# Optimization experiments

Measured on AMD Instinct MI355X. Metric: run time of the kernel, lower is better.

## Reference

```python
import jax, jax.numpy as jnp
import numpy as np

B, T1, T2, V, D, H = 128, 256, 256, 50000, 300, 300


def _lstm_dir(x, lens, Wih, Whh, bih, bhh):
    # PyTorch LSTM gate order: i, f, g, o. Length-masked scan emulates pack_padded_sequence:
    # state frozen and outputs zeroed for t >= len.
    Bn, T, _ = x.shape
    Hn = Whh.shape[1]
    mask = (jnp.arange(T)[None, :] < lens[:, None]).astype(x.dtype)[..., None]  # [B,T,1]

    def step(carry, inp):
        h, c = carry
        xt, mt = inp
        gates = xt @ Wih.T + bih + h @ Whh.T + bhh
        i, f, g, o = jnp.split(gates, 4, axis=-1)
        c_new = jax.nn.sigmoid(f) * c + jax.nn.sigmoid(i) * jnp.tanh(g)
        h_new = jax.nn.sigmoid(o) * jnp.tanh(c_new)
        h = mt * h_new + (1.0 - mt) * h
        c = mt * c_new + (1.0 - mt) * c
        return (h, c), h * mt

    init = (jnp.zeros((Bn, Hn), x.dtype), jnp.zeros((Bn, Hn), x.dtype))
    _, ys = jax.lax.scan(step, init, (x.swapaxes(0, 1), mask.swapaxes(0, 1)))
    return ys.swapaxes(0, 1)  # [B,T,H]


def _bilstm(x, lens, Wf_ih, Wf_hh, bf_ih, bf_hh, Wb_ih, Wb_hh, bb_ih, bb_hh):
    out_f = _lstm_dir(x, lens, Wf_ih, Wf_hh, bf_ih, bf_hh)
    T = x.shape[1]
    t = jnp.arange(T)[None, :]
    # per-sample reversal of the valid prefix (involution): rev[t] = l-1-t for t<l else t
    idx = jnp.where(t < lens[:, None], lens[:, None] - 1 - t, t)
    xr = jnp.take_along_axis(x, idx[..., None], axis=1)
    yr = _lstm_dir(xr, lens, Wb_ih, Wb_hh, bb_ih, bb_hh)
    out_b = jnp.take_along_axis(yr, idx[..., None], axis=1)
    return jnp.concatenate([out_f, out_b], axis=-1)  # [B,T,2H]


def _bidaf_both(u1, l1, u2, l2):
    S = jnp.einsum('bid,bjd->bij', u1, u2)  # [B,t1,t2]
    v1 = jnp.arange(S.shape[1])[None, :] < l1[:, None]
    v2 = jnp.arange(S.shape[2])[None, :] < l2[:, None]
    Sm = jnp.where(v1[:, :, None] & v2[:, None, :], S, -1e9)
    # softmax over t2 (s1->s2 attention); invalid rows zeroed (matches NaN->0 fill)
    a2 = jax.nn.softmax(Sm, axis=2) * v1[:, :, None].astype(S.dtype)
    a1 = jax.nn.softmax(Sm, axis=1) * v2[:, None, :].astype(S.dtype)
    U = jnp.einsum('bij,bjd->bid', a2, u2)   # tile for s1
    U1 = jnp.einsum('bij,bid->bjd', a1, u1)  # tile for s2
    return U, U1


def _max_along_time(x, lens):
    v = jnp.arange(x.shape[1])[None, :] < lens[:, None]
    return jnp.max(jnp.where(v[:, :, None], x, -jnp.inf), axis=1)


def _forward(s1, l1, s2, l2, emb,
             w1f_ih, w1f_hh, b1f_ih, b1f_hh, w1b_ih, w1b_hh, b1b_ih, b1b_hh,
             w2f_ih, w2f_hh, b2f_ih, b2f_hh, w2b_ih, w2b_hh, b2b_ih, b2b_hh,
             projW, projB, mlpW, mlpB, smW, smB):
    p1 = emb[s1]  # [B,T1,D]
    p2 = emb[s2]
    u1 = _bilstm(p1, l1, w1f_ih, w1f_hh, b1f_ih, b1f_hh, w1b_ih, w1b_hh, b1b_ih, b1b_hh)
    u2 = _bilstm(p2, l2, w1f_ih, w1f_hh, b1f_ih, b1f_hh, w1b_ih, w1b_hh, b1b_ih, b1b_hh)
    A1, A2 = _bidaf_both(u1, l1, u2, l2)
    c1 = jnp.concatenate([u1, A1, u1 - A1, u1 * A1], axis=-1)  # [B,T1,8H]
    c2 = jnp.concatenate([u2, A2, u2 - A2, u2 * A2], axis=-1)
    p1c = jax.nn.relu(c1 @ projW.T + projB)
    p2c = jax.nn.relu(c2 @ projW.T + projB)
    y1 = _bilstm(p1c, l1, w2f_ih, w2f_hh, b2f_ih, b2f_hh, w2b_ih, w2b_hh, b2b_ih, b2b_hh)
    y2 = _bilstm(p2c, l2, w2f_ih, w2f_hh, b2f_ih, b2f_hh, w2b_ih, w2b_hh, b2b_ih, b2b_hh)
    m1 = _max_along_time(y1, l1)  # [B,2H]
    m2 = _max_along_time(y2, l2)
    feat = jnp.concatenate([m1, m2, jnp.abs(m1 - m2), m1 * m2], axis=-1)  # [B,8H]
    h = jax.nn.relu(feat @ mlpW.T + mlpB)
    return h @ smW.T + smB  # [B,3]


def setup_inputs():
    key = jax.random.key(0)
    ks = jax.random.split(key, 24)
    sc = 0.05
    W = lambda i, shape: jax.random.normal(ks[i], shape, jnp.float32) * sc
    return dict(
        s1=jax.random.randint(ks[0], (B, T1), 0, V),
        l1=jax.random.randint(ks[1], (B,), 1, T1 + 1),
        s2=jax.random.randint(ks[2], (B, T2), 0, V),
        l2=jax.random.randint(ks[3], (B,), 1, T2 + 1),
        emb=W(4, (V, D)),
        w1f_ih=W(5, (4 * H, D)), w1f_hh=W(6, (4 * H, H)), b1f_ih=W(7, (4 * H,)), b1f_hh=W(8, (4 * H,)),
        w1b_ih=W(9, (4 * H, D)), w1b_hh=W(10, (4 * H, H)), b1b_ih=W(11, (4 * H,)), b1b_hh=W(12, (4 * H,)),
        w2f_ih=W(13, (4 * H, H)), w2f_hh=W(14, (4 * H, H)), b2f_ih=W(15, (4 * H,)), b2f_hh=W(16, (4 * H,)),
        w2b_ih=W(17, (4 * H, H)), w2b_hh=W(18, (4 * H, H)), b2b_ih=W(19, (4 * H,)), b2b_hh=W(20, (4 * H,)),
        projW=W(21, (H, 8 * H)), projB=jnp.zeros((H,), jnp.float32),
        mlpW=W(22, (300, 8 * H)), mlpB=jnp.zeros((300,), jnp.float32),
        smW=W(23, (3, 300)), smB=jnp.zeros((3,), jnp.float32),
    )


def reference(s1, l1, s2, l2, emb,
              w1f_ih, w1f_hh, b1f_ih, b1f_hh, w1b_ih, w1b_hh, b1b_ih, b1b_hh,
              w2f_ih, w2f_hh, b2f_ih, b2f_hh, w2b_ih, w2b_hh, b2b_ih, b2b_hh,
              projW, projB, mlpW, mlpB, smW, smB):
    return _forward(s1, l1, s2, l2, emb,
                    w1f_ih, w1f_hh, b1f_ih, b1f_hh, w1b_ih, w1b_hh, b1b_ih, b1b_hh,
                    w2f_ih, w2f_hh, b2f_ih, b2f_hh, w2b_ih, w2b_hh, b2b_ih, b2b_hh,
                    projW, projB, mlpW, mlpB, smW, smB)
```

## Files before the change

### kernel.cpp

```cpp
#include <hip/hip_runtime.h>
#include <hip/hip_bf16.h>


typedef unsigned short u16;
typedef float fx4 __attribute__((ext_vector_type(4)));
typedef short s16x8 __attribute__((ext_vector_type(8)));

__device__ __forceinline__ float us2f(u16 u){
  unsigned int x = ((unsigned int)u) << 16;
  float f; __builtin_memcpy(&f, &x, 4); return f;
}
__device__ __forceinline__ u16 f2us(float f){
  unsigned int x; __builtin_memcpy(&x, &f, 4);
  unsigned int r = x + 0x7fffu + ((x >> 16) & 1u);
  return (u16)(r >> 16);
}
__device__ __forceinline__ float sigmf(float x){ return 1.0f/(1.0f + __expf(-x)); }
__device__ __forceinline__ float tanhfast(float x){ return 1.0f - 2.0f/(__expf(2.0f*x) + 1.0f); }

__global__ __launch_bounds__(256) void k_embed(const int* __restrict__ s1, const int* __restrict__ s2,
                                               const float* __restrict__ emb, u16* __restrict__ p)
{
  int id = blockIdx.x*256 + threadIdx.x;
  if (id >= 65536*75) return;
  int row = id / 75;
  int c4 = (id - row*75) * 4;
  int tok = (row < 32768) ? s1[row] : s2[row - 32768];
  float4 v = *(const float4*)(emb + (size_t)tok*300 + c4);
  ushort4 o; o.x=f2us(v.x); o.y=f2us(v.y); o.z=f2us(v.z); o.w=f2us(v.w);
  *(ushort4*)(p + (size_t)row*300 + c4) = o;
}

__global__ __launch_bounds__(256) void k_cvt(const float* __restrict__ in, u16* __restrict__ out, int n)
{
  int id = blockIdx.x*256 + threadIdx.x;
  if (id < n) out[id] = f2us(in[id]);
}

__global__ __launch_bounds__(256) void k_pack(const float* __restrict__ W, u16* __restrict__ pack)
{
  int id = blockIdx.x*256 + threadIdx.x;
  if (id >= 51200) return;
  const int lane = id & 63;
  const int kt2 = (id >> 6) % 10;
  const int nt2 = id / 640;
  const int n = nt2*16 + (lane & 15);
  u16 tmp[8];
#pragma unroll
  for (int j = 0; j < 8; ++j){
    const int k = kt2*32 + (lane >> 4)*8 + j;
    tmp[j] = (n < 1200 && k < 300) ? f2us(W[(size_t)n*300 + k]) : (u16)0;
  }
  *(s16x8*)(pack + (size_t)id*8) = *(const s16x8*)tmp;
}

__global__ __launch_bounds__(256) void k_mm_xpc(
    const u16* __restrict__ A,
    const u16* __restrict__ WFb, const u16* __restrict__ WBb,
    const float* __restrict__ bF1, const float* __restrict__ bF2,
    const float* __restrict__ bB1, const float* __restrict__ bB2,
    const int* __restrict__ l1, const int* __restrict__ l2,
    u16* __restrict__ xp, int c)
{
  const int dir = blockIdx.z;
  const u16* Bw = dir ? WBb : WFb;
  const float* b1 = dir ? bB1 : bF1;
  const float* b2 = dir ? bB2 : bF2;
  u16* xpd = xp + (size_t)dir*9830400;
  __shared__ u16 As[128][40];
  __shared__ u16 Bs[128][40];
  const int tid = threadIdx.x;
  const int m0 = blockIdx.y << 7;
  const int n0 = blockIdx.x << 7;
  const int srow0 = tid >> 2;
  const int kcol = (tid & 3) << 3;
  int src[2];
#pragma unroll
  for (int p = 0; p < 2; ++p){
    const int row = srow0 + (p << 6);
    const int ml = m0 + row;
    const int r = ml >> 5, tl = ml & 31;
    const int L = (r < 128) ? l1[r] : l2[r-128];
    const int tg = (c << 5) + tl;
    const int s = dir ? ((tg < L) ? (L-1-tg) : tg) : tg;
    src[p] = r*256 + s;
  }
  const int wv = tid >> 6;
  const int wm = (wv >> 1) << 6, wn = (wv & 1) << 6;
  const int lq = (tid >> 4) & 3;
  const int lr = tid & 15;
  fx4 acc[4][4];
#pragma unroll
  for (int i = 0; i < 4; ++i)
#pragma unroll
    for (int j = 0; j < 4; ++j) acc[i][j] = (fx4){0.f,0.f,0.f,0.f};

  for (int kt = 0; kt < 10; ++kt){
    const int k = (kt << 5) + kcol;
#pragma unroll
    for (int p = 0; p < 2; ++p){
      u16 tmp[8];
      const u16* ap = A + (size_t)src[p]*300 + k;
      if (k + 8 <= 300){
        *(ushort4*)&tmp[0] = *(const ushort4*)ap;
        *(ushort4*)&tmp[4] = *(const ushort4*)(ap + 4);
      } else {
#pragma unroll
        for (int j = 0; j < 8; ++j) tmp[j] = (k + j < 300) ? ap[j] : (u16)0;
      }
      *(s16x8*)&As[srow0 + (p << 6)][kcol] = *(const s16x8*)tmp;

      const int n = n0 + srow0 + (p << 6);
      u16 tmb[8] = {0,0,0,0,0,0,0,0};
      if (n < 1200){
        const u16* bp = Bw + (size_t)n*300 + k;
        if (k + 8 <= 300){
          *(ushort4*)&tmb[0] = *(const ushort4*)bp;
          *(ushort4*)&tmb[4] = *(const ushort4*)(bp + 4);
        } else {
#pragma unroll
          for (int j = 0; j < 8; ++j) tmb[j] = (k + j < 300) ? bp[j] : (u16)0;
        }
      }
      *(s16x8*)&Bs[srow0 + (p << 6)][kcol] = *(const s16x8*)tmb;
    }
    __syncthreads();
    s16x8 af[4], bf[4];
#pragma unroll
    for (int mi = 0; mi < 4; ++mi) af[mi] = *(const s16x8*)&As[wm + mi*16 + lr][lq << 3];
#pragma unroll
    for (int ni = 0; ni < 4; ++ni) bf[ni] = *(const s16x8*)&Bs[wn + ni*16 + lr][lq << 3];
#pragma unroll
    for (int mi = 0; mi < 4; ++mi)
#pragma unroll
      for (int ni = 0; ni < 4; ++ni)
        acc[mi][ni] = __builtin_amdgcn_mfma_f32_16x16x32_bf16(af[mi], bf[ni], acc[mi][ni], 0, 0, 0);
    __syncthreads();
  }
#pragma unroll
  for (int ni = 0; ni < 4; ++ni){
    const int n = n0 + wn + ni*16 + lr;
    if (n < 1200){
      const float bias = b1[n] + b2[n];
#pragma unroll
      for (int mi = 0; mi < 4; ++mi){
        const int m = m0 + wm + mi*16 + (lq << 2);
#pragma unroll
        for (int reg = 0; reg < 4; ++reg)
          xpd[(size_t)(m + reg)*1200 + n] = f2us(acc[mi][ni][reg] + bias);
      }
    }
  }
}

__global__ __launch_bounds__(256) void k_mm_s(const u16* __restrict__ U, float* __restrict__ S)
{
  __shared__ u16 As[128][40];
  __shared__ u16 Bs[128][40];
  const int tid = threadIdx.x;
  const int bz = blockIdx.z;
  const u16* Ap = U + (size_t)bz*153600;
  const u16* Bp = U + (size_t)(128+bz)*153600;
  float* C = S + (size_t)bz*65536;
  const int m0 = blockIdx.y << 7;
  const int n0 = blockIdx.x << 7;
  const int srow0 = tid >> 2;
  const int kcol = (tid & 3) << 3;
  const int wv = tid >> 6;
  const int wm = (wv >> 1) << 6, wn = (wv & 1) << 6;
  const int lq = (tid >> 4) & 3;
  const int lr = tid & 15;
  fx4 acc[4][4];
#pragma unroll
  for (int i = 0; i < 4; ++i)
#pragma unroll
    for (int j = 0; j < 4; ++j) acc[i][j] = (fx4){0.f,0.f,0.f,0.f};

  for (int kt = 0; kt < 19; ++kt){
    const int k = (kt << 5) + kcol;
#pragma unroll
    for (int p = 0; p < 2; ++p){
      const int row = srow0 + (p << 6);
      u16 tma[8] = {0,0,0,0,0,0,0,0};
      u16 tmb[8] = {0,0,0,0,0,0,0,0};
      if (k + 8 <= 600){
        *(s16x8*)tma = *(const s16x8*)(Ap + (size_t)(m0 + row)*600 + k);
        *(s16x8*)tmb = *(const s16x8*)(Bp + (size_t)(n0 + row)*600 + k);
      }
      *(s16x8*)&As[row][kcol] = *(const s16x8*)tma;
      *(s16x8*)&Bs[row][kcol] = *(const s16x8*)tmb;
    }
    __syncthreads();
    s16x8 af[4], bf[4];
#pragma unroll
    for (int mi = 0; mi < 4; ++mi) af[mi] = *(const s16x8*)&As[wm + mi*16 + lr][lq << 3];
#pragma unroll
    for (int ni = 0; ni < 4; ++ni) bf[ni] = *(const s16x8*)&Bs[wn + ni*16 + lr][lq << 3];
#pragma unroll
    for (int mi = 0; mi < 4; ++mi)
#pragma unroll
      for (int ni = 0; ni < 4; ++ni)
        acc[mi][ni] = __builtin_amdgcn_mfma_f32_16x16x32_bf16(af[mi], bf[ni], acc[mi][ni], 0, 0, 0);
    __syncthreads();
  }
#pragma unroll
  for (int mi = 0; mi < 4; ++mi){
    const int m = m0 + wm + mi*16 + (lq << 2);
#pragma unroll
    for (int ni = 0; ni < 4; ++ni){
      const int n = n0 + wn + ni*16 + lr;
#pragma unroll
      for (int reg = 0; reg < 4; ++reg)
        C[(size_t)(m + reg)*256 + n] = acc[mi][ni][reg];
    }
  }
}

__global__ __launch_bounds__(256) void k_mm_proj(
    const u16* __restrict__ U, const u16* __restrict__ ATT,
    const u16* __restrict__ Bw,
    const float* __restrict__ bias,
    u16* __restrict__ C)
{
  __shared__ u16 As0[128][40];
  __shared__ u16 As1[128][40];
  __shared__ u16 Bs0[128][40];
  __shared__ u16 Bs1[128][40];
  const int tid = threadIdx.x;
  const int id = ((int)(blockIdx.x & 7))*192 + ((int)blockIdx.x >> 3);
  const int mg = id / 3, nb = id - mg*3;
  const int m0 = mg << 7, n0 = nb << 7;
  const int srow0 = tid >> 2;
  const int kcol = (tid & 3) << 3;
  const int wv = tid >> 6;
  const int wm = (wv >> 1) << 6, wn = (wv & 1) << 6;
  const int lq = (tid >> 4) & 3;
  const int lr = tid & 15;
  fx4 acc[4][4];
#pragma unroll
  for (int i = 0; i < 4; ++i)
#pragma unroll
    for (int j = 0; j < 4; ++j) acc[i][j] = (fx4){0.f,0.f,0.f,0.f};

  for (int kt = 0; kt < 19; ++kt){
    const int off = (kt << 5) + kcol;
    const bool ok = (off < 600);
#pragma unroll
    for (int p = 0; p < 2; ++p){
      const int row = srow0 + (p << 6);
      u16 u8[8] = {0,0,0,0,0,0,0,0};
      u16 a8[8] = {0,0,0,0,0,0,0,0};
      if (ok){
        *(s16x8*)u8 = *(const s16x8*)(U   + (size_t)(m0+row)*600 + off);
        *(s16x8*)a8 = *(const s16x8*)(ATT + (size_t)(m0+row)*600 + off);
      }
      *(s16x8*)&As0[row][kcol] = *(const s16x8*)u8;
      *(s16x8*)&As1[row][kcol] = *(const s16x8*)a8;
      const int n = n0 + row;
      u16 w0[8] = {0,0,0,0,0,0,0,0};
      u16 w1[8] = {0,0,0,0,0,0,0,0};
      if (n < 300 && ok){
        *(s16x8*)w0 = *(const s16x8*)(Bw + (size_t)n*2400 + off);
        *(s16x8*)w1 = *(const s16x8*)(Bw + (size_t)n*2400 + 600 + off);
      }
      *(s16x8*)&Bs0[row][kcol] = *(const s16x8*)w0;
      *(s16x8*)&Bs1[row][kcol] = *(const s16x8*)w1;
    }
    __syncthreads();
    {
      s16x8 af0[4], af1[4], bf0[4], bf1[4];
#pragma unroll
      for (int mi = 0; mi < 4; ++mi){
        af0[mi] = *(const s16x8*)&As0[wm + mi*16 + lr][lq << 3];
        af1[mi] = *(const s16x8*)&As1[wm + mi*16 + lr][lq << 3];
      }
#pragma unroll
      for (int ni = 0; ni < 4; ++ni){
        bf0[ni] = *(const s16x8*)&Bs0[wn + ni*16 + lr][lq << 3];
        bf1[ni] = *(const s16x8*)&Bs1[wn + ni*16 + lr][lq << 3];
      }
#pragma unroll
      for (int mi = 0; mi < 4; ++mi)
#pragma unroll
        for (int ni = 0; ni < 4; ++ni){
          acc[mi][ni] = __builtin_amdgcn_mfma_f32_16x16x32_bf16(af0[mi], bf0[ni], acc[mi][ni], 0, 0, 0);
          acc[mi][ni] = __builtin_amdgcn_mfma_f32_16x16x32_bf16(af1[mi], bf1[ni], acc[mi][ni], 0, 0, 0);
        }
    }
    __syncthreads();
#pragma unroll
    for (int p = 0; p < 2; ++p){
      const int row = srow0 + (p << 6);
      u16 u8[8] = {0,0,0,0,0,0,0,0};
      u16 a8[8] = {0,0,0,0,0,0,0,0};
      if (ok){
        *(s16x8*)u8 = *(const s16x8*)(U   + (size_t)(m0+row)*600 + off);
        *(s16x8*)a8 = *(const s16x8*)(ATT + (size_t)(m0+row)*600 + off);
      }
      u16 d8[8], m8[8];
#pragma unroll
      for (int j = 0; j < 8; ++j){
        const float uf = us2f(u8[j]), af = us2f(a8[j]);
        d8[j] = f2us(uf - af);
        m8[j] = f2us(uf * af);
      }
      *(s16x8*)&As0[row][kcol] = *(const s16x8*)d8;
      *(s16x8*)&As1[row][kcol] = *(const s16x8*)m8;
      const int n = n0 + row;
      u16 w2[8] = {0,0,0,0,0,0,0,0};
      u16 w3[8] = {0,0,0,0,0,0,0,0};
      if (n < 300 && ok){
        *(s16x8*)w2 = *(const s16x8*)(Bw + (size_t)n*2400 + 1200 + off);
        *(s16x8*)w3 = *(const s16x8*)(Bw + (size_t)n*2400 + 1800 + off);
      }
      *(s16x8*)&Bs0[row][kcol] = *(const s16x8*)w2;
      *(s16x8*)&Bs1[row][kcol] = *(const s16x8*)w3;
    }
    __syncthreads();
    {
      s16x8 af0[4], af1[4], bf0[4], bf1[4];
#pragma unroll
      for (int mi = 0; mi < 4; ++mi){
        af0[mi] = *(const s16x8*)&As0[wm + mi*16 + lr][lq << 3];
        af1[mi] = *(const s16x8*)&As1[wm + mi*16 + lr][lq << 3];
      }
#pragma unroll
      for (int ni = 0; ni < 4; ++ni){
        bf0[ni] = *(const s16x8*)&Bs0[wn + ni*16 + lr][lq << 3];
        bf1[ni] = *(const s16x8*)&Bs1[wn + ni*16 + lr][lq << 3];
      }
#pragma unroll
      for (int mi = 0; mi < 4; ++mi)
#pragma unroll
        for (int ni = 0; ni < 4; ++ni){
          acc[mi][ni] = __builtin_amdgcn_mfma_f32_16x16x32_bf16(af0[mi], bf0[ni], acc[mi][ni], 0, 0, 0);
          acc[mi][ni] = __builtin_amdgcn_mfma_f32_16x16x32_bf16(af1[mi], bf1[ni], acc[mi][ni], 0, 0, 0);
        }
    }
    __syncthreads();
  }
#pragma unroll
  for (int ni = 0; ni < 4; ++ni){
    const int n = n0 + wn + ni*16 + lr;
    if (n < 300){
      const float bs = bias[n];
#pragma unroll
      for (int mi = 0; mi < 4; ++mi){
        const int m = m0 + wm + mi*16 + (lq << 2);
#pragma unroll
        for (int reg = 0; reg < 4; ++reg)
          C[(size_t)(m + reg)*300 + n] = f2us(fmaxf(acc[mi][ni][reg] + bs, 0.0f));
      }
    }
  }
}

__global__ __launch_bounds__(512) void k_scan_mf(
    const u16* __restrict__ xp,
    const u16* __restrict__ packF, const u16* __restrict__ packB,
    const int* __restrict__ l1, const int* __restrict__ l2,
    u16* __restrict__ uo,
    u16* __restrict__ hG, float* __restrict__ cG,
    int c)
{
  __shared__ u16 h_pack[10][64][8];
  __shared__ float gs[8][1200];
  __shared__ u16 wring[8][3][4][512];
  __shared__ int L_s[8];
  const int bid = blockIdx.x;
  const int dir = bid & 1, sg = bid >> 1;
  const int r0 = sg << 3;
  const u16* pack = dir ? packB : packF;
  const u16* xpd = xp + (size_t)dir*9830400;
  const int tid = threadIdx.x;
  if (tid < 8) L_s[tid] = (r0 + tid < 128) ? l1[r0 + tid] : l2[r0 + tid - 128];
  for (int i = tid; i < 10*64*8; i += 512) ((u16*)h_pack)[i] = 0;
  __syncthreads();
  if (c > 0){
    for (int i = tid; i < 2400; i += 512){
      const int q = i / 300, d = i - q*300;
      h_pack[d >> 5][(((d & 31) >> 3) << 4) | q][d & 7] =
          hG[(size_t)(dir*256 + r0 + q)*328 + d];
    }
  }
  int q_[5], d_[5]; bool v_[5];
#pragma unroll
  for (int j = 0; j < 5; ++j){
    const int u0 = tid + (j << 9);
    v_[j] = (u0 < 2400);
    const int qq = v_[j] ? (u0 / 300) : 0;
    q_[j] = qq;
    d_[j] = v_[j] ? (u0 - qq*300) : 0;
  }
  float c_reg[5];
#pragma unroll
  for (int j = 0; j < 5; ++j)
    c_reg[j] = (v_[j] && c > 0) ? cG[(size_t)(dir*256 + r0 + q_[j])*304 + d_[j]] : 0.0f;
  __syncthreads();

  int Lmax = 0;
#pragma unroll
  for (int q = 0; q < 8; ++q) Lmax = max(Lmax, L_s[q]);
  const int t0 = c << 5;
  int nts = Lmax - t0; if (nts > 32) nts = 32;
  if (nts <= 0) return;

  const int w = tid >> 6, lane = tid & 63;
  const int lq = lane >> 4, lr = lane & 15;
  const int tile0 = w * 10;
  const u16* pw = pack + (size_t)tile0*5120;
  const unsigned wb0 = (unsigned)(uintptr_t)&wring[w][0][0][0] + (unsigned)lane*16u;

#define WISSUE(FB, BUF)                                                                  \
  {                                                                                      \
    _Pragma("unroll")                                                                    \
    for (int i2 = 0; i2 < 4; ++i2){                                                      \
      const int f_ = (FB) + i2;                                                          \
      const u16* ga = pw + ((size_t)(((f_ % 10)*10) + (f_ / 10)))*512 + (size_t)lane*8;  \
      __builtin_amdgcn_global_load_lds(                                                  \
        (const __attribute__((address_space(1))) void*)ga,                               \
        (__attribute__((address_space(3))) void*)&wring[w][BUF][i2][0], 16, 0, 0);       \
    }                                                                                    \
  }

  WISSUE(0, 0)
  WISSUE(4, 1)
  int rot = 0;

  for (int tl = 0; tl < nts; ++tl){
    const int t = t0 + tl;
    const int bsel0 = rot;
    const int bsel1 = (rot + 1 == 3) ? 0 : rot + 1;
    const int bsel2 = (rot + 2 >= 3) ? rot - 1 : rot + 2;
    const int bsel[3] = { bsel0, bsel1, bsel2 };
    __builtin_amdgcn_sched_barrier(0);
    u16 xg0[5], xg1[5], xg2[5], xg3[5];
#pragma unroll
    for (int j = 0; j < 5; ++j){
      const size_t base = (size_t)((r0 + q_[j])*32 + tl)*1200 + d_[j];
      xg0[j] = v_[j] ? xpd[base      ] : (u16)0;
      xg1[j] = v_[j] ? xpd[base + 300] : (u16)0;
      xg2[j] = v_[j] ? xpd[base + 600] : (u16)0;
      xg3[j] = v_[j] ? xpd[base + 900] : (u16)0;
    }
    __builtin_amdgcn_sched_barrier(0);

    fx4 acc[10];
#pragma unroll
    for (int nt = 0; nt < 10; ++nt) acc[nt] = (fx4){0.f,0.f,0.f,0.f};

#pragma unroll
    for (int p = 0; p < 25; ++p){
      if (p < 2){ asm volatile("s_waitcnt vmcnt(24)" ::: "memory"); }
      else      { asm volatile("s_waitcnt vmcnt(4)"  ::: "memory"); }
      __builtin_amdgcn_sched_barrier(0);
      const unsigned ab = wb0 + (unsigned)bsel[p % 3]*4096u;
      s16x8 b0, b1, b2, b3;
      asm volatile("ds_read_b128 %0, %1"             : "=v"(b0) : "v"(ab));
      asm volatile("ds_read_b128 %0, %1 offset:1024" : "=v"(b1) : "v"(ab));
      asm volatile("ds_read_b128 %0, %1 offset:2048" : "=v"(b2) : "v"(ab));
      asm volatile("ds_read_b128 %0, %1 offset:3072" : "=v"(b3) : "v"(ab));
      const int kt0 = (4*p) / 10;
      const int kt3 = (4*p + 3) / 10;
      const s16x8 a0 = *(const s16x8*)&h_pack[kt0][lane][0];
      const s16x8 a1 = (kt3 != kt0) ? *(const s16x8*)&h_pack[kt3][lane][0] : a0;
      WISSUE((((p + 2) % 25) * 4), bsel[(p + 2) % 3])
      asm volatile("s_waitcnt lgkmcnt(0)" ::: "memory");
      __builtin_amdgcn_sched_barrier(0);
      {
        const int f0 = 4*p;
        acc[(f0+0) % 10] = __builtin_amdgcn_mfma_f32_16x16x32_bf16(((f0+0)/10 == kt0) ? a0 : a1, b0, acc[(f0+0) % 10], 0, 0, 0);
        acc[(f0+1) % 10] = __builtin_amdgcn_mfma_f32_16x16x32_bf16(((f0+1)/10 == kt0) ? a0 : a1, b1, acc[(f0+1) % 10], 0, 0, 0);
        acc[(f0+2) % 10] = __builtin_amdgcn_mfma_f32_16x16x32_bf16(((f0+2)/10 == kt0) ? a0 : a1, b2, acc[(f0+2) % 10], 0, 0, 0);
        acc[(f0+3) % 10] = __builtin_amdgcn_mfma_f32_16x16x32_bf16(((f0+3)/10 == kt0) ? a0 : a1, b3, acc[(f0+3) % 10], 0, 0, 0);
      }
    }
    rot = (rot + 1 == 3) ? 0 : rot + 1;

    if (lq < 2){
#pragma unroll
      for (int nt = 0; nt < 10; ++nt){
        const int n = (tile0 + nt)*16 + lr;
        if (n < 1200){
#pragma unroll
          for (int reg = 0; reg < 4; ++reg)
            gs[(lq << 2) + reg][n] = acc[nt][reg];
        }
      }
    }
    asm volatile("s_waitcnt lgkmcnt(0)" ::: "memory");
    __builtin_amdgcn_sched_barrier(0);
    __builtin_amdgcn_s_barrier();
#pragma unroll
    for (int j = 0; j < 5; ++j){
      if (v_[j]){
        const int q = q_[j], d = d_[j];
        const int L = L_s[q];
        if (t < L){
          const float gi = gs[q][d]       + us2f(xg0[j]);
          const float gf = gs[q][300 + d] + us2f(xg1[j]);
          const float gg = gs[q][600 + d] + us2f(xg2[j]);
          const float go = gs[q][900 + d] + us2f(xg3[j]);
          const float cn = sigmf(gf)*c_reg[j] + sigmf(gi)*tanhfast(gg);
          const float hn = sigmf(go)*tanhfast(cn);
          c_reg[j] = cn;
          const u16 hb = f2us(hn);
          h_pack[d >> 5][(((d & 31) >> 3) << 4) | q][d & 7] = hb;
          const int wpos = dir ? (L-1-t) : t;
          uo[(size_t)((r0 + q)*256 + wpos)*600 + dir*300 + d] = hb;
        }
      }
    }
    asm volatile("s_waitcnt lgkmcnt(0)" ::: "memory");
    __builtin_amdgcn_sched_barrier(0);
    __builtin_amdgcn_s_barrier();
  }
#undef WISSUE
  for (int i = tid; i < 2400; i += 512){
    const int q = i / 300, d = i - q*300;
    hG[(size_t)(dir*256 + r0 + q)*328 + d] =
        h_pack[d >> 5][(((d & 31) >> 3) << 4) | q][d & 7];
  }
#pragma unroll
  for (int j = 0; j < 5; ++j)
    if (v_[j]) cG[(size_t)(dir*256 + r0 + q_[j])*304 + d_[j]] = c_reg[j];
}

__global__ __launch_bounds__(256) void k_row_stats(const float* __restrict__ S, const int* __restrict__ l2,
                                                   float* __restrict__ rmax, float* __restrict__ rinv)
{
  const int wid = threadIdx.x >> 6, lane = threadIdx.x & 63;
  const int row = blockIdx.x*4 + wid;
  const int b = row >> 8;
  const int L2b = l2[b];
  float4 v = *(const float4*)(S + (size_t)row*256 + lane*4);
  const int j = lane*4;
  float m = -INFINITY;
  if (j   < L2b) m = fmaxf(m, v.x);
  if (j+1 < L2b) m = fmaxf(m, v.y);
  if (j+2 < L2b) m = fmaxf(m, v.z);
  if (j+3 < L2b) m = fmaxf(m, v.w);
  for (int off = 32; off; off >>= 1) m = fmaxf(m, __shfl_xor(m, off));
  float s = 0.f;
  if (j   < L2b) s += __expf(v.x - m);
  if (j+1 < L2b) s += __expf(v.y - m);
  if (j+2 < L2b) s += __expf(v.z - m);
  if (j+3 < L2b) s += __expf(v.w - m);
  for (int off = 32; off; off >>= 1) s += __shfl_xor(s, off);
  if (lane == 0){ rmax[row] = m; rinv[row] = 1.0f/s; }
}

__global__ __launch_bounds__(256) void k_col_stats(const float* __restrict__ S, const int* __restrict__ l1,
                                                   float* __restrict__ cmax, float* __restrict__ cinv)
{
  const int b = blockIdx.x;
  const int j = threadIdx.x;
  const int L1b = l1[b];
  const float* Sb = S + (size_t)b*65536;
  float m = -INFINITY;
  for (int i = 0; i < L1b; ++i) m = fmaxf(m, Sb[(size_t)i*256 + j]);
  float s = 0.f;
  for (int i = 0; i < L1b; ++i) s += __expf(Sb[(size_t)i*256 + j] - m);
  cmax[b*256 + j] = m;
  cinv[b*256 + j] = 1.0f/s;
}

__global__ __launch_bounds__(256) void k_av_row(
    const float* __restrict__ S, const u16* __restrict__ U,
    const int* __restrict__ l1, const int* __restrict__ l2,
    const float* __restrict__ rmax, const float* __restrict__ rinv,
    u16* __restrict__ ATT)
{
  __shared__ float Ps[32][68];
  __shared__ float Us[32][68];
  const int tid = threadIdx.x;
  const int b = blockIdx.z;
  const int i0 = blockIdx.y << 6;
  const int d0 = blockIdx.x << 6;
  const int L1b = l1[b], L2b = l2[b];
  const float* Sb = S + (size_t)b*65536;
  const u16* u2 = U + (size_t)(128+b)*153600;
  const int tx = tid & 15, ty = tid >> 4;
  float acc[4][4];
#pragma unroll
  for (int i = 0; i < 4; ++i)
#pragma unroll
    for (int j = 0; j < 4; ++j) acc[i][j] = 0.0f;

  for (int kt = 0; kt < 8; ++kt){
    const int j0 = kt << 5;
#pragma unroll
    for (int q = 0; q < 2; ++q){
      const int f4 = tid + (q << 8);
      {
        const int row = f4 >> 3;
        const int c4 = (f4 & 7) << 2;
        const int i = i0 + row;
        float4 s4 = *(const float4*)(Sb + (size_t)i*256 + j0 + c4);
        const float rm = rmax[(b<<8) + i];
        const float ri = rinv[(b<<8) + i];
        const int jb = j0 + c4;
        Ps[c4  ][row] = (jb   < L2b) ? __expf(s4.x - rm)*ri : 0.0f;
        Ps[c4+1][row] = (jb+1 < L2b) ? __expf(s4.y - rm)*ri : 0.0f;
        Ps[c4+2][row] = (jb+2 < L2b) ? __expf(s4.z - rm)*ri : 0.0f;
        Ps[c4+3][row] = (jb+3 < L2b) ? __expf(s4.w - rm)*ri : 0.0f;
      }
      {
        const int row = f4 >> 4;
        const int c4 = (f4 & 15) << 2;
        const int d = d0 + c4;
        float4 v = make_float4(0.f,0.f,0.f,0.f);
        if (j0 + row < L2b){
          const u16* up = u2 + (size_t)(j0+row)*600 + d;
          if (d + 3 < 600){
            ushort4 t4 = *(const ushort4*)up;
            v.x=us2f(t4.x); v.y=us2f(t4.y); v.z=us2f(t4.z); v.w=us2f(t4.w);
          } else {
            if (d   < 600) v.x = us2f(up[0]);
            if (d+1 < 600) v.y = us2f(up[1]);
            if (d+2 < 600) v.z = us2f(up[2]);
          }
        }
        *(float4*)&Us[row][c4] = v;
      }
    }
    __syncthreads();
#pragma unroll
    for (int kk = 0; kk < 32; ++kk){
      float4 a = *(const float4*)&Ps[kk][ty<<2];
      float4 bb = *(const float4*)&Us[kk][tx<<2];
      float av[4] = {a.x,a.y,a.z,a.w};
      float bv[4] = {bb.x,bb.y,bb.z,bb.w};
#pragma unroll
      for (int ii = 0; ii < 4; ++ii)
#pragma unroll
        for (int jj = 0; jj < 4; ++jj)
          acc[ii][jj] = fmaf(av[ii], bv[jj], acc[ii][jj]);
    }
    __syncthreads();
  }
#pragma unroll
  for (int ii = 0; ii < 4; ++ii){
    const int i = i0 + (ty<<2) + ii;
#pragma unroll
    for (int jj = 0; jj < 4; ++jj){
      const int d = d0 + (tx<<2) + jj;
      if (d < 600)
        ATT[(size_t)b*153600 + (size_t)i*600 + d] = f2us((i < L1b) ? acc[ii][jj] : 0.0f);
    }
  }
}

__global__ __launch_bounds__(256) void k_av_col(
    const float* __restrict__ S, const u16* __restrict__ U,
    const int* __restrict__ l1, const int* __restrict__ l2,
    const float* __restrict__ cmax, const float* __restrict__ cinv,
    u16* __restrict__ ATT)
{
  __shared__ float Ps[32][68];
  __shared__ float Us[32][68];
  const int tid = threadIdx.x;
  const int b = blockIdx.z;
  const int j0v = blockIdx.y << 6;
  const int d0 = blockIdx.x << 6;
  const int L1b = l1[b], L2b = l2[b];
  const float* Sb = S + (size_t)b*65536;
  const u16* u1 = U + (size_t)b*153600;
  const int tx = tid & 15, ty = tid >> 4;
  float acc[4][4];
#pragma unroll
  for (int i = 0; i < 4; ++i)
#pragma unroll
    for (int j = 0; j < 4; ++j) acc[i][j] = 0.0f;

  for (int kt = 0; kt < 8; ++kt){
    const int i0k = kt << 5;
#pragma unroll
    for (int q = 0; q < 2; ++q){
      const int f4 = tid + (q << 8);
      const int row = f4 >> 4;
      const int c4 = (f4 & 15) << 2;
      {
        const int i = i0k + row;
        const int j = j0v + c4;
        float4 s4 = *(const float4*)(Sb + (size_t)i*256 + j);
        const bool iok = i < L1b;
        Ps[row][c4  ] = iok ? __expf(s4.x - cmax[(b<<8)+j  ])*cinv[(b<<8)+j  ] : 0.0f;
        Ps[row][c4+1] = iok ? __expf(s4.y - cmax[(b<<8)+j+1])*cinv[(b<<8)+j+1] : 0.0f;
        Ps[row][c4+2] = iok ? __expf(s4.z - cmax[(b<<8)+j+2])*cinv[(b<<8)+j+2] : 0.0f;
        Ps[row][c4+3] = iok ? __expf(s4.w - cmax[(b<<8)+j+3])*cinv[(b<<8)+j+3] : 0.0f;
      }
      {
        const int d = d0 + c4;
        float4 v = make_float4(0.f,0.f,0.f,0.f);
        if (i0k + row < L1b){
          const u16* up = u1 + (size_t)(i0k+row)*600 + d;
          if (d + 3 < 600){
            ushort4 t4 = *(const ushort4*)up;
            v.x=us2f(t4.x); v.y=us2f(t4.y); v.z=us2f(t4.z); v.w=us2f(t4.w);
          } else {
            if (d   < 600) v.x = us2f(up[0]);
            if (d+1 < 600) v.y = us2f(up[1]);
            if (d+2 < 600) v.z = us2f(up[2]);
          }
        }
        *(float4*)&Us[row][c4] = v;
      }
    }
    __syncthreads();
#pragma unroll
    for (int kk = 0; kk < 32; ++kk){
      float4 a = *(const float4*)&Ps[kk][ty<<2];
      float4 bb = *(const float4*)&Us[kk][tx<<2];
      float av[4] = {a.x,a.y,a.z,a.w};
      float bv[4] = {bb.x,bb.y,bb.z,bb.w};
#pragma unroll
      for (int ii = 0; ii < 4; ++ii)
#pragma unroll
        for (int jj = 0; jj < 4; ++jj)
          acc[ii][jj] = fmaf(av[ii], bv[jj], acc[ii][jj]);
    }
    __syncthreads();
  }
#pragma unroll
  for (int ii = 0; ii < 4; ++ii){
    const int j = j0v + (ty<<2) + ii;
#pragma unroll
    for (int jj = 0; jj < 4; ++jj){
      const int d = d0 + (tx<<2) + jj;
      if (d < 600)
        ATT[(size_t)(128+b)*153600 + (size_t)j*600 + d] = f2us((j < L2b) ? acc[ii][jj] : 0.0f);
    }
  }
}

__global__ __launch_bounds__(256) void k_maxfeat(const u16* __restrict__ y,
                                                 const int* __restrict__ l1, const int* __restrict__ l2,
                                                 float* __restrict__ feat)
{
  const int b = blockIdx.x;
  const int La = l1[b], Lb = l2[b];
  for (int c = threadIdx.x; c < 600; c += 256){
    float m1 = -INFINITY, m2 = -INFINITY;
    const u16* y1 = y + (size_t)b*153600 + c;
    for (int t = 0; t < La; ++t) m1 = fmaxf(m1, us2f(y1[(size_t)t*600]));
    const u16* y2 = y + (size_t)(128+b)*153600 + c;
    for (int t = 0; t < Lb; ++t) m2 = fmaxf(m2, us2f(y2[(size_t)t*600]));
    feat[(size_t)b*2400 + c]        = m1;
    feat[(size_t)b*2400 + 600 + c]  = m2;
    feat[(size_t)b*2400 + 1200 + c] = fabsf(m1 - m2);
    feat[(size_t)b*2400 + 1800 + c] = m1*m2;
  }
}

__global__ __launch_bounds__(256) void k_rowgemm(const float* __restrict__ feat, const float* __restrict__ W,
                                                 const float* __restrict__ bias, float* __restrict__ out)
{
  const int b = blockIdx.x;
  __shared__ float ff[2400];
  for (int i = threadIdx.x; i < 2400; i += 256) ff[i] = feat[(size_t)b*2400 + i];
  __syncthreads();
  for (int n = threadIdx.x; n < 300; n += 256){
    const float* w = W + (size_t)n*2400;
    float acc = bias[n];
    for (int k = 0; k < 2400; k += 4){
      float4 wv = *(const float4*)(w + k);
      acc += ff[k]*wv.x + ff[k+1]*wv.y + ff[k+2]*wv.z + ff[k+3]*wv.w;
    }
    out[(size_t)b*300 + n] = fmaxf(acc, 0.0f);
  }
}

__global__ __launch_bounds__(192) void k_final(const float* __restrict__ h, const float* __restrict__ smW,
                                               const float* __restrict__ smB, float* __restrict__ out)
{
  const int b = blockIdx.x;
  const int n = threadIdx.x >> 6, lane = threadIdx.x & 63;
  float acc = 0.f;
  for (int k = lane; k < 300; k += 64) acc += h[(size_t)b*300 + k]*smW[(size_t)n*300 + k];
  for (int off = 32; off; off >>= 1) acc += __shfl_xor(acc, off);
  if (lane == 0) out[b*3 + n] = acc + smB[n];
}

extern "C" void kernel_launch(void* const* d_in, const int* in_sizes, int n_in,
                              void* d_out, int out_size, void* d_ws, size_t ws_size,
                              hipStream_t stream)
{
  (void)in_sizes; (void)n_in; (void)out_size;
  static const size_t OFF_P  = 0;
  static const size_t OFF_B  = 39321600;
  static const size_t OFF_U  = 78643200;
  static const size_t OFF_D  = 157286400;
  static const size_t OFF_WT = 235929600;
  static const size_t OFF_PJ = 238809600;
  static const size_t OFF_PK = 240249600;
  static const size_t OFF_ST = 243526400;
  static const size_t OFF_FE = 244050688;
  static const size_t OFF_HM = 245279488;
  static const size_t OFF_HC = 245433088;
  static const size_t WS_NEEDED = 246391552;
  if (ws_size < WS_NEEDED) return;

  const int* s1 = (const int*)d_in[0];
  const int* l1 = (const int*)d_in[1];
  const int* s2 = (const int*)d_in[2];
  const int* l2 = (const int*)d_in[3];
  const float* emb    = (const float*)d_in[4];
  const float* w1f_ih = (const float*)d_in[5];
  const float* w1f_hh = (const float*)d_in[6];
  const float* b1f_ih = (const float*)d_in[7];
  const float* b1f_hh = (const float*)d_in[8];
  const float* w1b_ih = (const float*)d_in[9];
  const float* w1b_hh = (const float*)d_in[10];
  const float* b1b_ih = (const float*)d_in[11];
  const float* b1b_hh = (const float*)d_in[12];
  const float* w2f_ih = (const float*)d_in[13];
  const float* w2f_hh = (const float*)d_in[14];
  const float* b2f_ih = (const float*)d_in[15];
  const float* b2f_hh = (const float*)d_in[16];
  const float* w2b_ih = (const float*)d_in[17];
  const float* w2b_hh = (const float*)d_in[18];
  const float* b2b_ih = (const float*)d_in[19];
  const float* b2b_hh = (const float*)d_in[20];
  const float* projW  = (const float*)d_in[21];
  const float* projB  = (const float*)d_in[22];
  const float* mlpW   = (const float*)d_in[23];
  const float* mlpB   = (const float*)d_in[24];
  const float* smW    = (const float*)d_in[25];
  const float* smB    = (const float*)d_in[26];

  char* ws = (char*)d_ws;
  u16*   p    = (u16*)(ws + OFF_P);
  u16*   xp1  = (u16*)(ws + OFF_B);
  float* Smat = (float*)(ws + OFF_B);
  u16*   pc   = (u16*)(ws + OFF_B);
  u16*   uu   = (u16*)(ws + OFF_U);
  u16*   att  = (u16*)(ws + OFF_D);
  u16*   xp2  = (u16*)(ws + OFF_D);
  u16*   wih  = (u16*)(ws + OFF_WT);
  u16*   pjw  = (u16*)(ws + OFF_PJ);
  u16*   pk   = (u16*)(ws + OFF_PK);
  float* st   = (float*)(ws + OFF_ST);
  float* feat = (float*)(ws + OFF_FE);
  float* hml  = (float*)(ws + OFF_HM);
  u16*   hG   = (u16*)(ws + OFF_HC);
  float* cG   = (float*)(ws + OFF_HC + 335872);

  k_embed<<<19200, 256, 0, stream>>>(s1, s2, emb, p);
  k_cvt<<<1407, 256, 0, stream>>>(w1f_ih, wih,           360000);
  k_cvt<<<1407, 256, 0, stream>>>(w1b_ih, wih + 360000,  360000);
  k_cvt<<<1407, 256, 0, stream>>>(w2f_ih, wih + 720000,  360000);
  k_cvt<<<1407, 256, 0, stream>>>(w2b_ih, wih + 1080000, 360000);
  k_cvt<<<2813, 256, 0, stream>>>(projW,  pjw,           720000);
  k_pack<<<200, 256, 0, stream>>>(w1f_hh, pk);
  k_pack<<<200, 256, 0, stream>>>(w1b_hh, pk + 409600);
  k_pack<<<200, 256, 0, stream>>>(w2f_hh, pk + 819200);
  k_pack<<<200, 256, 0, stream>>>(w2b_hh, pk + 1228800);

  const dim3 gxp(10, 64, 2);
  for (int c = 0; c < 8; ++c){
    k_mm_xpc<<<gxp, 256, 0, stream>>>(p, wih, wih + 360000, b1f_ih, b1f_hh, b1b_ih, b1b_hh,
                                      l1, l2, xp1, c);
    k_scan_mf<<<64, 512, 0, stream>>>(xp1, pk, pk + 409600, l1, l2, uu, hG, cG, c);
  }

  k_mm_s<<<dim3(2,2,128), 256, 0, stream>>>(uu, Smat);
  k_row_stats<<<8192, 256, 0, stream>>>(Smat, l2, st, st + 32768);
  k_col_stats<<<128, 256, 0, stream>>>(Smat, l1, st + 65536, st + 98304);
  k_av_row<<<dim3(10,4,128), 256, 0, stream>>>(Smat, uu, l1, l2, st, st + 32768, att);
  k_av_col<<<dim3(10,4,128), 256, 0, stream>>>(Smat, uu, l1, l2, st + 65536, st + 98304, att);

  k_mm_proj<<<1536, 256, 0, stream>>>(uu, att, pjw, projB, pc);

  for (int c = 0; c < 8; ++c){
    k_mm_xpc<<<gxp, 256, 0, stream>>>(pc, wih + 720000, wih + 1080000, b2f_ih, b2f_hh, b2b_ih, b2b_hh,
                                      l1, l2, xp2, c);
    k_scan_mf<<<64, 512, 0, stream>>>(xp2, pk + 819200, pk + 1228800, l1, l2, uu, hG, cG, c);
  }

  k_maxfeat<<<128, 256, 0, stream>>>(uu, l1, l2, feat);
  k_rowgemm<<<128, 256, 0, stream>>>(feat, mlpW, mlpB, hml);
  k_final<<<128, 192, 0, stream>>>(hml, smW, smB, (float*)d_out);
}
```

Before: 9.869 ms.

## Process 16 rows per scan block with 1024 threads and register-streamed weights

The recurrent LSTM scan now handles 16 sequences per block, filling all 16 MFMA M-rows instead of 8. It uses 1024 threads across 16 waves, each covering 5 gate tiles instead of 10, and launches half as many blocks. The LDS weight ring fed by global_load_lds is removed, and recurrent weights are loaded straight from global into registers with a two-stage register double buffer. The input-projection loads move from a prefetch ahead of the MFMA loop into the gate update. The aim is to halve per-row weight traffic and shorten the serial MFMA chain per step, at the cost of exposing global-load latency each timestep and using fewer CUs.

```diff
diff --git a/kernel.cpp b/kernel.cpp
--- a/kernel.cpp
+++ b/kernel.cpp
@@ -355,7 +355,7 @@
   }
 }
 
-__global__ __launch_bounds__(512) void k_scan_mf(
+__global__ __launch_bounds__(1024) void k_scan_mf(
     const u16* __restrict__ xp,
     const u16* __restrict__ packF, const u16* __restrict__ packB,
     const int* __restrict__ l1, const int* __restrict__ l2,
@@ -364,143 +364,100 @@
     int c)
 {
   __shared__ u16 h_pack[10][64][8];
-  __shared__ float gs[8][1200];
-  __shared__ u16 wring[8][3][4][512];
-  __shared__ int L_s[8];
+  __shared__ float gs[16][1200];
+  __shared__ int L_s[16];
   const int bid = blockIdx.x;
   const int dir = bid & 1, sg = bid >> 1;
-  const int r0 = sg << 3;
+  const int r0 = sg << 4;
   const u16* pack = dir ? packB : packF;
   const u16* xpd = xp + (size_t)dir*9830400;
   const int tid = threadIdx.x;
-  if (tid < 8) L_s[tid] = (r0 + tid < 128) ? l1[r0 + tid] : l2[r0 + tid - 128];
-  for (int i = tid; i < 10*64*8; i += 512) ((u16*)h_pack)[i] = 0;
+  if (tid < 16) L_s[tid] = (r0 + tid < 128) ? l1[r0 + tid] : l2[r0 + tid - 128];
+  for (int i = tid; i < 10*64*8; i += 1024) ((u16*)h_pack)[i] = 0;
   __syncthreads();
   if (c > 0){
-    for (int i = tid; i < 2400; i += 512){
+    for (int i = tid; i < 4800; i += 1024){
       const int q = i / 300, d = i - q*300;
       h_pack[d >> 5][(((d & 31) >> 3) << 4) | q][d & 7] =
           hG[(size_t)(dir*256 + r0 + q)*328 + d];
     }
   }
-  int q_[5], d_[5]; bool v_[5];
+  float c_reg[5];
 #pragma unroll
   for (int j = 0; j < 5; ++j){
-    const int u0 = tid + (j << 9);
-    v_[j] = (u0 < 2400);
-    const int qq = v_[j] ? (u0 / 300) : 0;
-    q_[j] = qq;
-    d_[j] = v_[j] ? (u0 - qq*300) : 0;
-  }
-  float c_reg[5];
-#pragma unroll
-  for (int j = 0; j < 5; ++j)
-    c_reg[j] = (v_[j] && c > 0) ? cG[(size_t)(dir*256 + r0 + q_[j])*304 + d_[j]] : 0.0f;
+    const int u0 = tid + (j << 10);
+    float v = 0.0f;
+    if (u0 < 4800 && c > 0){
+      const int q = u0 / 300, d = u0 - q*300;
+      v = cG[(size_t)(dir*256 + r0 + q)*304 + d];
+    }
+    c_reg[j] = v;
+  }
   __syncthreads();
-
   int Lmax = 0;
 #pragma unroll
-  for (int q = 0; q < 8; ++q) Lmax = max(Lmax, L_s[q]);
+  for (int q = 0; q < 16; ++q) Lmax = max(Lmax, L_s[q]);
   const int t0 = c << 5;
   int nts = Lmax - t0; if (nts > 32) nts = 32;
   if (nts <= 0) return;
 
   const int w = tid >> 6, lane = tid & 63;
   const int lq = lane >> 4, lr = lane & 15;
-  const int tile0 = w * 10;
-  const u16* pw = pack + (size_t)tile0*5120;
-  const unsigned wb0 = (unsigned)(uintptr_t)&wring[w][0][0][0] + (unsigned)lane*16u;
-
-#define WISSUE(FB, BUF)                                                                  \
-  {                                                                                      \
-    _Pragma("unroll")                                                                    \
-    for (int i2 = 0; i2 < 4; ++i2){                                                      \
-      const int f_ = (FB) + i2;                                                          \
-      const u16* ga = pw + ((size_t)(((f_ % 10)*10) + (f_ / 10)))*512 + (size_t)lane*8;  \
-      __builtin_amdgcn_global_load_lds(                                                  \
-        (const __attribute__((address_space(1))) void*)ga,                               \
-        (__attribute__((address_space(3))) void*)&wring[w][BUF][i2][0], 16, 0, 0);       \
-    }                                                                                    \
-  }
-
-  WISSUE(0, 0)
-  WISSUE(4, 1)
-  int rot = 0;
+  const int tile0 = w * 5;
+  const u16* pw = pack + (size_t)tile0*5120 + (size_t)lane*8;
 
   for (int tl = 0; tl < nts; ++tl){
     const int t = t0 + tl;
-    const int bsel0 = rot;
-    const int bsel1 = (rot + 1 == 3) ? 0 : rot + 1;
-    const int bsel2 = (rot + 2 >= 3) ? rot - 1 : rot + 2;
-    const int bsel[3] = { bsel0, bsel1, bsel2 };
-    __builtin_amdgcn_sched_barrier(0);
-    u16 xg0[5], xg1[5], xg2[5], xg3[5];
+    fx4 acc[5];
+#pragma unroll
+    for (int i = 0; i < 5; ++i) acc[i] = (fx4){0.f,0.f,0.f,0.f};
+    s16x8 wA[5], wB[5];
+#pragma unroll
+    for (int i = 0; i < 5; ++i) wA[i] = *(const s16x8*)(pw + (size_t)(i*10 + 0)*512);
+#pragma unroll
+    for (int ktp = 0; ktp < 5; ++ktp){
+      const int ktE = 2*ktp, ktO = ktE + 1;
+#pragma unroll
+      for (int i = 0; i < 5; ++i) wB[i] = *(const s16x8*)(pw + (size_t)(i*10 + ktO)*512);
+      {
+        const s16x8 a = *(const s16x8*)&h_pack[ktE][lane][0];
+#pragma unroll
+        for (int i = 0; i < 5; ++i)
+          acc[i] = __builtin_amdgcn_mfma_f32_16x16x32_bf16(a, wA[i], acc[i], 0, 0, 0);
+      }
+      if (ktp < 4){
+#pragma unroll
+        for (int i = 0; i < 5; ++i) wA[i] = *(const s16x8*)(pw + (size_t)(i*10 + ktE + 2)*512);
+      }
+      {
+        const s16x8 a = *(const s16x8*)&h_pack[ktO][lane][0];
+#pragma unroll
+        for (int i = 0; i < 5; ++i)
+          acc[i] = __builtin_amdgcn_mfma_f32_16x16x32_bf16(a, wB[i], acc[i], 0, 0, 0);
+      }
+    }
+#pragma unroll
+    for (int i = 0; i < 5; ++i){
+      const int n = (tile0 + i)*16 + lr;
+      if (n < 1200){
+#pragma unroll
+        for (int reg = 0; reg < 4; ++reg)
+          gs[(lq << 2) + reg][n] = acc[i][reg];
+      }
+    }
+    __syncthreads();
 #pragma unroll
     for (int j = 0; j < 5; ++j){
-      const size_t base = (size_t)((r0 + q_[j])*32 + tl)*1200 + d_[j];
-      xg0[j] = v_[j] ? xpd[base      ] : (u16)0;
-      xg1[j] = v_[j] ? xpd[base + 300] : (u16)0;
-      xg2[j] = v_[j] ? xpd[base + 600] : (u16)0;
-      xg3[j] = v_[j] ? xpd[base + 900] : (u16)0;
-    }
-    __builtin_amdgcn_sched_barrier(0);
-
-    fx4 acc[10];
-#pragma unroll
-    for (int nt = 0; nt < 10; ++nt) acc[nt] = (fx4){0.f,0.f,0.f,0.f};
-
-#pragma unroll
-    for (int p = 0; p < 25; ++p){
-      if (p < 2){ asm volatile("s_waitcnt vmcnt(24)" ::: "memory"); }
-      else      { asm volatile("s_waitcnt vmcnt(4)"  ::: "memory"); }
-      __builtin_amdgcn_sched_barrier(0);
-      const unsigned ab = wb0 + (unsigned)bsel[p % 3]*4096u;
-      s16x8 b0, b1, b2, b3;
-      asm volatile("ds_read_b128 %0, %1"             : "=v"(b0) : "v"(ab));
-      asm volatile("ds_read_b128 %0, %1 offset:1024" : "=v"(b1) : "v"(ab));
-      asm volatile("ds_read_b128 %0, %1 offset:2048" : "=v"(b2) : "v"(ab));
-      asm volatile("ds_read_b128 %0, %1 offset:3072" : "=v"(b3) : "v"(ab));
-      const int kt0 = (4*p) / 10;
-      const int kt3 = (4*p + 3) / 10;
-      const s16x8 a0 = *(const s16x8*)&h_pack[kt0][lane][0];
-      const s16x8 a1 = (kt3 != kt0) ? *(const s16x8*)&h_pack[kt3][lane][0] : a0;
-      WISSUE((((p + 2) % 25) * 4), bsel[(p + 2) % 3])
-      asm volatile("s_waitcnt lgkmcnt(0)" ::: "memory");
-      __builtin_amdgcn_sched_barrier(0);
-      {
-        const int f0 = 4*p;
-        acc[(f0+0) % 10] = __builtin_amdgcn_mfma_f32_16x16x32_bf16(((f0+0)/10 == kt0) ? a0 : a1, b0, acc[(f0+0) % 10], 0, 0, 0);
-        acc[(f0+1) % 10] = __builtin_amdgcn_mfma_f32_16x16x32_bf16(((f0+1)/10 == kt0) ? a0 : a1, b1, acc[(f0+1) % 10], 0, 0, 0);
-        acc[(f0+2) % 10] = __builtin_amdgcn_mfma_f32_16x16x32_bf16(((f0+2)/10 == kt0) ? a0 : a1, b2, acc[(f0+2) % 10], 0, 0, 0);
-        acc[(f0+3) % 10] = __builtin_amdgcn_mfma_f32_16x16x32_bf16(((f0+3)/10 == kt0) ? a0 : a1, b3, acc[(f0+3) % 10], 0, 0, 0);
-      }
-    }
-    rot = (rot + 1 == 3) ? 0 : rot + 1;
-
-    if (lq < 2){
-#pragma unroll
-      for (int nt = 0; nt < 10; ++nt){
-        const int n = (tile0 + nt)*16 + lr;
-        if (n < 1200){
-#pragma unroll
-          for (int reg = 0; reg < 4; ++reg)
-            gs[(lq << 2) + reg][n] = acc[nt][reg];
-        }
-      }
-    }
-    asm volatile("s_waitcnt lgkmcnt(0)" ::: "memory");
-    __builtin_amdgcn_sched_barrier(0);
-    __builtin_amdgcn_s_barrier();
-#pragma unroll
-    for (int j = 0; j < 5; ++j){
-      if (v_[j]){
-        const int q = q_[j], d = d_[j];
+      const int u0 = tid + (j << 10);
+      if (u0 < 4800){
+        const int q = u0 / 300, d = u0 - q*300;
         const int L = L_s[q];
         if (t < L){
-          const float gi = gs[q][d]       + us2f(xg0[j]);
-          const float gf = gs[q][300 + d] + us2f(xg1[j]);
-          const float gg = gs[q][600 + d] + us2f(xg2[j]);
-          const float go = gs[q][900 + d] + us2f(xg3[j]);
+          const size_t xb = (size_t)((r0 + q)*32 + tl)*1200 + d;
+          const float gi = gs[q][d]       + us2f(xpd[xb      ]);
+          const float gf = gs[q][300 + d] + us2f(xpd[xb + 300]);
+          const float gg = gs[q][600 + d] + us2f(xpd[xb + 600]);
+          const float go = gs[q][900 + d] + us2f(xpd[xb + 900]);
           const float cn = sigmf(gf)*c_reg[j] + sigmf(gi)*tanhfast(gg);
           const float hn = sigmf(go)*tanhfast(cn);
           c_reg[j] = cn;
@@ -511,19 +468,21 @@
         }
       }
     }
-    asm volatile("s_waitcnt lgkmcnt(0)" ::: "memory");
-    __builtin_amdgcn_sched_barrier(0);
-    __builtin_amdgcn_s_barrier();
-  }
-#undef WISSUE
-  for (int i = tid; i < 2400; i += 512){
+    __syncthreads();
+  }
+  for (int i = tid; i < 4800; i += 1024){
     const int q = i / 300, d = i - q*300;
     hG[(size_t)(dir*256 + r0 + q)*328 + d] =
         h_pack[d >> 5][(((d & 31) >> 3) << 4) | q][d & 7];
   }
 #pragma unroll
-  for (int j = 0; j < 5; ++j)
-    if (v_[j]) cG[(size_t)(dir*256 + r0 + q_[j])*304 + d_[j]] = c_reg[j];
+  for (int j = 0; j < 5; ++j){
+    const int u0 = tid + (j << 10);
+    if (u0 < 4800){
+      const int q = u0 / 300, d = u0 - q*300;
+      cG[(size_t)(dir*256 + r0 + q)*304 + d] = c_reg[j];
+    }
+  }
 }
 
 __global__ __launch_bounds__(256) void k_row_stats(const float* __restrict__ S, const int* __restrict__ l2,
@@ -861,7 +820,7 @@
   for (int c = 0; c < 8; ++c){
     k_mm_xpc<<<gxp, 256, 0, stream>>>(p, wih, wih + 360000, b1f_ih, b1f_hh, b1b_ih, b1b_hh,
                                       l1, l2, xp1, c);
-    k_scan_mf<<<64, 512, 0, stream>>>(xp1, pk, pk + 409600, l1, l2, uu, hG, cG, c);
+    k_scan_mf<<<32, 1024, 0, stream>>>(xp1, pk, pk + 409600, l1, l2, uu, hG, cG, c);
   }
 
   k_mm_s<<<dim3(2,2,128), 256, 0, stream>>>(uu, Smat);
@@ -875,7 +834,7 @@
   for (int c = 0; c < 8; ++c){
     k_mm_xpc<<<gxp, 256, 0, stream>>>(pc, wih + 720000, wih + 1080000, b2f_ih, b2f_hh, b2b_ih, b2b_hh,
                                       l1, l2, xp2, c);
-    k_scan_mf<<<64, 512, 0, stream>>>(xp2, pk + 819200, pk + 1228800, l1, l2, uu, hG, cG, c);
+    k_scan_mf<<<32, 1024, 0, stream>>>(xp2, pk + 819200, pk + 1228800, l1, l2, uu, hG, cG, c);
   }
 
   k_maxfeat<<<128, 256, 0, stream>>>(uu, l1, l2, feat);
```

New measurement: 12.15 ms. +23.1%, slower.
